# Performance work log

Measured on AMD Instinct MI355X. Metric: run time of the kernel, lower is better.

The kernel has to match this reference:

```python
import jax, jax.numpy as jnp
import numpy as np

N, E = 50000, 800000
NODE_DIM, HIDDEN, NBASIS = 128, 128, 32


def _mlp(x, w1, b1, w2, b2):
    return jax.nn.silu(x @ w1 + b1) @ w2 + b2


def setup_inputs() -> dict:
    key = jax.random.key(0)
    ks = jax.random.split(key, 16)
    d = {}
    d['h'] = jax.random.normal(ks[0], (N, NODE_DIM), dtype=jnp.float32)
    d['pos'] = jax.random.normal(ks[1], (N, 3), dtype=jnp.float32)
    d['edge_index'] = jax.random.randint(ks[2], (2, E), 0, N, dtype=jnp.int32)
    mlp_in = NODE_DIM * 2 + NBASIS
    def lin(k, fan_in, fan_out):
        bound = 1.0 / np.sqrt(fan_in)
        kw, kb = jax.random.split(k)
        w = jax.random.uniform(kw, (fan_in, fan_out), minval=-bound, maxval=bound, dtype=jnp.float32)
        b = jax.random.uniform(kb, (fan_out,), minval=-bound, maxval=bound, dtype=jnp.float32)
        return w, b
    d['mw1'], d['mb1'] = lin(ks[3], mlp_in, HIDDEN)
    d['mw2'], d['mb2'] = lin(ks[4], HIDDEN, HIDDEN)
    d['nw1'], d['nb1'] = lin(ks[5], NODE_DIM + HIDDEN, HIDDEN)
    d['nw2'], d['nb2'] = lin(ks[6], HIDDEN, NODE_DIM)
    d['cw1'], d['cb1'] = lin(ks[7], HIDDEN, HIDDEN)
    d['cw2'], d['cb2'] = lin(ks[8], HIDDEN, 1)
    return d


def reference(h, pos, edge_index, mw1, mb1, mw2, mb2, nw1, nb1, nw2, nb2, cw1, cb1, cw2, cb2):
    row, col = edge_index[0], edge_index[1]
    # Gaussian smearing constants (start=0, stop=10, num_gaussians=NBASIS)
    offset = jnp.linspace(0.0, 10.0, NBASIS)  # [NBASIS]
    coeff = -0.5 / float(10.0 / (NBASIS - 1)) ** 2

    rel_pos = pos[row] - pos[col]                       # [E, 3]
    sq_dist = jnp.sum(rel_pos ** 2, axis=1, keepdims=True)  # [E, 1]
    dist = jnp.sqrt(sq_dist + 1e-8)                     # [E, 1]
    dist_emb = jnp.exp(coeff * (dist - offset[None, :]) ** 2)  # [E, NBASIS]

    msg_in = jnp.concatenate([h[row], h[col], dist_emb], axis=1)  # [E, 2D+NBASIS]
    messages = _mlp(msg_in, mw1, mb1, mw2, mb2)         # [E, HIDDEN]

    aggr_msgs = jax.ops.segment_sum(messages, row, num_segments=h.shape[0])  # [N, HIDDEN]

    coord_mult = _mlp(messages, cw1, cb1, cw2, cb2)     # [E, 1]
    coord_updates = rel_pos * coord_mult                # [E, 3]
    aggr_coord = jax.ops.segment_sum(coord_updates, row, num_segments=pos.shape[0])
    pos_out = pos + aggr_coord

    node_in = jnp.concatenate([h, aggr_msgs], axis=1)   # [N, D+HIDDEN]
    h_out = h + _mlp(node_in, nw1, nb1, nw2, nb2)
    return (h_out, pos_out)
```

## Files before the change

kernel.cpp:

```cpp
#include <hip/hip_runtime.h>
#include <math.h>

#define N_NODES 50000
#define E_EDGES 800000
#define D 128
#define HID 128
#define NB 32
#define SCAN_BLOCKS 196

typedef __attribute__((ext_vector_type(8))) short bf16x8;
typedef __attribute__((ext_vector_type(4))) float f32x4;

#define MW1F 0
#define MW2F 72
#define CW1F 104
#define NW1F 136
#define NW2F 200
#define TOT_KSTEPS 29

__device__ __forceinline__ short f2bf(float f) {
    union { float f; unsigned u; } v; v.f = f;
    unsigned r = v.u + 0x7fffu + ((v.u >> 16) & 1u);
    return (short)(r >> 16);
}
__device__ __forceinline__ float bf2f(unsigned s) {
    union { unsigned u; float f; } v; v.u = s << 16; return v.f;
}
__device__ __forceinline__ float silu_f(float x) { return x / (1.0f + __expf(-x)); }
__device__ __forceinline__ f32x4 splat4(float b) { f32x4 v = {b, b, b, b}; return v; }

__global__ void pack_w(const float* __restrict__ mw1, const float* __restrict__ mw2,
                       const float* __restrict__ cw1, const float* __restrict__ nw1,
                       const float* __restrict__ nw2, short* __restrict__ wp)
{
    const int bid = blockIdx.x;
    const int ks = bid >> 3, nf = bid & 7;
    const int l = threadIdx.x;
    const float* src; int k0;
    if (ks < 9)       { src = mw1; k0 = ks; }
    else if (ks < 13) { src = mw2; k0 = ks - 9; }
    else if (ks < 17) { src = cw1; k0 = ks - 13; }
    else if (ks < 25) { src = nw1; k0 = ks - 17; }
    else              { src = nw2; k0 = ks - 25; }
    bf16x8 pv;
    #pragma unroll
    for (int j = 0; j < 8; ++j)
        pv[j] = f2bf(src[(size_t)(k0 * 32 + (l >> 4) * 8 + j) * 128 + nf * 16 + (l & 15)]);
    *((bf16x8*)wp + (size_t)bid * 64 + l) = pv;
}

__global__ void conv_h(const float* __restrict__ h, short* __restrict__ hb)
{
    int i = blockIdx.x * 256 + threadIdx.x;
    if (i < N_NODES * D / 8) {
        float4 va = ((const float4*)h)[i * 2];
        float4 vb = ((const float4*)h)[i * 2 + 1];
        bf16x8 o;
        o[0] = f2bf(va.x); o[1] = f2bf(va.y); o[2] = f2bf(va.z); o[3] = f2bf(va.w);
        o[4] = f2bf(vb.x); o[5] = f2bf(vb.y); o[6] = f2bf(vb.z); o[7] = f2bf(vb.w);
        ((bf16x8*)hb)[i] = o;
    }
}

__global__ void count_rows(const int* __restrict__ ei, int* __restrict__ cnt)
{
    int e = blockIdx.x * 256 + threadIdx.x;
    if (e < E_EDGES) atomicAdd(&cnt[ei[e]], 1);
}

__global__ void scan_blocks(const int* __restrict__ cnt, int* __restrict__ base,
                            int* __restrict__ bsum)
{
    __shared__ int wsum[4];
    const int t = threadIdx.x, b = blockIdx.x;
    const int i = b * 256 + t;
    int v = (i < N_NODES) ? cnt[i] : 0;
    int incl = v;
    #pragma unroll
    for (int off = 1; off < 64; off <<= 1) {
        int u = __shfl_up(incl, off);
        if ((t & 63) >= off) incl += u;
    }
    if ((t & 63) == 63) wsum[t >> 6] = incl;
    __syncthreads();
    int wo = 0;
    #pragma unroll
    for (int wv = 0; wv < 4; ++wv) if (wv < (t >> 6)) wo += wsum[wv];
    if (i < N_NODES) base[i] = wo + incl - v;
    if (t == 255) bsum[b] = wo + incl;
}

__global__ void scan_bsums(const int* __restrict__ bsum, int* __restrict__ boff)
{
    __shared__ int wsum[4];
    const int t = threadIdx.x;
    int v = (t < SCAN_BLOCKS) ? bsum[t] : 0;
    int incl = v;
    #pragma unroll
    for (int off = 1; off < 64; off <<= 1) {
        int u = __shfl_up(incl, off);
        if ((t & 63) >= off) incl += u;
    }
    if ((t & 63) == 63) wsum[t >> 6] = incl;
    __syncthreads();
    int wo = 0;
    #pragma unroll
    for (int wv = 0; wv < 4; ++wv) if (wv < (t >> 6)) wo += wsum[wv];
    if (t < SCAN_BLOCKS) boff[t] = wo + incl - v;
}

__global__ void add_offsets(int* __restrict__ base, const int* __restrict__ boff,
                            int* __restrict__ fill)
{
    int i = blockIdx.x * 256 + threadIdx.x;
    if (i < N_NODES) {
        int v = base[i] + boff[blockIdx.x];
        base[i] = v; fill[i] = v;
    }
}

__global__ void scatter_edges(const int* __restrict__ ei, int* __restrict__ fill,
                              int* __restrict__ perm)
{
    int e = blockIdx.x * 256 + threadIdx.x;
    if (e < E_EDGES) {
        int p = atomicAdd(&fill[ei[e]], 1);
        perm[p] = e;
    }
}

#define GEMM2(KSTEPS, STRIDE, WBASE)                                           \
    _Pragma("unroll")                                                          \
    for (int ks = 0; ks < KSTEPS; ++ks) {                                      \
        const int kd = ks * 32 + ag * 8;                                       \
        int b0 = ar * STRIDE + kd * 2;        b0 ^= (ar & 7) << 4;             \
        int b1 = (16 + ar) * STRIDE + kd * 2; b1 ^= (ar & 7) << 4;             \
        bf16x8 a0 = *(const bf16x8*)(sx + b0);                                 \
        bf16x8 a1 = *(const bf16x8*)(sx + b1);                                 \
        const bf16x8* bw = wpv + (size_t)(WBASE + ks * 8) * 64 + l;            \
        _Pragma("unroll")                                                      \
        for (int n = 0; n < 8; ++n) {                                          \
            bf16x8 bb = bw[n * 64];                                            \
            acc0[n] = __builtin_amdgcn_mfma_f32_16x16x32_bf16(a0, bb, acc0[n], 0, 0, 0); \
            acc1[n] = __builtin_amdgcn_mfma_f32_16x16x32_bf16(a1, bb, acc1[n], 0, 0, 0); \
        }                                                                      \
    }

template<int GATHER>
__global__ __launch_bounds__(128, 4) void egnn_edge(
    const short* __restrict__ hb, const float* __restrict__ pos,
    const int* __restrict__ ei, const int* __restrict__ perm,
    const float* __restrict__ mb1, const float* __restrict__ mb2,
    const float* __restrict__ cb1, const float* __restrict__ cw2,
    const float* __restrict__ cb2, const short* __restrict__ wp,
    float* __restrict__ aggr_msgs, float* __restrict__ aggr_coord,
    short* __restrict__ msgb, float* __restrict__ cu)
{
    __shared__ char  sm[2][8192];
    __shared__ int   s_row[2][32], s_col[2][32];
    __shared__ float s_dist[2][32];
    __shared__ float s_rel[2][32][3];

    const int t = threadIdx.x;
    const int w = t >> 6;
    const int l = t & 63;
    char* sx = sm[w];
    const bf16x8* wpv = (const bf16x8*)wp;
    const bf16x8* hbv = (const bf16x8*)hb;
    const int e0 = blockIdx.x * 64 + w * 32;

    if (l < 32) {
        const int ge = perm[e0 + l];
        const int row = ei[ge], col = ei[E_EDGES + ge];
        const float dx = pos[row * 3 + 0] - pos[col * 3 + 0];
        const float dy = pos[row * 3 + 1] - pos[col * 3 + 1];
        const float dz = pos[row * 3 + 2] - pos[col * 3 + 2];
        const float dist = sqrtf(dx * dx + dy * dy + dz * dz + 1e-8f);
        s_row[w][l] = row; s_col[w][l] = col; s_dist[w][l] = dist;
        s_rel[w][l][0] = dx; s_rel[w][l][1] = dy; s_rel[w][l][2] = dz;
    }
    asm volatile("s_waitcnt lgkmcnt(0)" ::: "memory");

    const int ar = l & 15, ag = l >> 4;
    const int row0 = s_row[w][ar],      col0 = s_col[w][ar];
    const int row1 = s_row[w][16 + ar], col1 = s_col[w][16 + ar];
    const float d0 = s_dist[w][ar], d1 = s_dist[w][16 + ar];

    const float GS = 10.0f / 31.0f;
    const float GC = -0.5f / (GS * GS);

    f32x4 acc0[8], acc1[8];

    #pragma unroll
    for (int n = 0; n < 8; ++n) {
        float b = mb1[n * 16 + ar];
        acc0[n] = splat4(b); acc1[n] = splat4(b);
    }
    #pragma unroll
    for (int ks = 0; ks < 9; ++ks) {
        bf16x8 a0, a1;
        if (ks < 4) {
            a0 = hbv[(size_t)row0 * 16 + ks * 4 + ag];
            a1 = hbv[(size_t)row1 * 16 + ks * 4 + ag];
        } else if (ks < 8) {
            a0 = hbv[(size_t)col0 * 16 + (ks - 4) * 4 + ag];
            a1 = hbv[(size_t)col1 * 16 + (ks - 4) * 4 + ag];
        } else {
            #pragma unroll
            for (int j = 0; j < 8; ++j) {
                const float g = (float)(ag * 8 + j) * GS;
                const float dd0 = d0 - g, dd1 = d1 - g;
                a0[j] = f2bf(__expf(GC * dd0 * dd0));
                a1[j] = f2bf(__expf(GC * dd1 * dd1));
            }
        }
        const bf16x8* bw = wpv + (size_t)(MW1F + ks * 8) * 64 + l;
        #pragma unroll
        for (int n = 0; n < 8; ++n) {
            bf16x8 bb = bw[n * 64];
            acc0[n] = __builtin_amdgcn_mfma_f32_16x16x32_bf16(a0, bb, acc0[n], 0, 0, 0);
            acc1[n] = __builtin_amdgcn_mfma_f32_16x16x32_bf16(a1, bb, acc1[n], 0, 0, 0);
        }
    }

    #pragma unroll
    for (int m = 0; m < 2; ++m)
        #pragma unroll
        for (int n = 0; n < 8; ++n)
            #pragma unroll
            for (int r = 0; r < 4; ++r) {
                float x = (m == 0) ? acc0[n][r] : acc1[n][r];
                const int rw = m * 16 + ag * 4 + r;
                const int cl = n * 16 + ar;
                int byte = rw * 256 + cl * 2;
                byte ^= (rw & 7) << 4;
                *(short*)(sx + byte) = f2bf(silu_f(x));
            }
    asm volatile("s_waitcnt lgkmcnt(0)" ::: "memory");

    #pragma unroll
    for (int n = 0; n < 8; ++n) {
        float b = mb2[n * 16 + ar];
        acc0[n] = splat4(b); acc1[n] = splat4(b);
    }
    GEMM2(4, 256, MW2F)

    int grows[2][4];
    #pragma unroll
    for (int m = 0; m < 2; ++m)
        #pragma unroll
        for (int r = 0; r < 4; ++r)
            grows[m][r] = s_row[w][m * 16 + ag * 4 + r];

    #pragma unroll
    for (int m = 0; m < 2; ++m)
        #pragma unroll
        for (int n = 0; n < 8; ++n)
            #pragma unroll
            for (int r = 0; r < 4; ++r) {
                float x = (m == 0) ? acc0[n][r] : acc1[n][r];
                const int rw = m * 16 + ag * 4 + r;
                const int cl = n * 16 + ar;
                int byte = rw * 256 + cl * 2;
                byte ^= (rw & 7) << 4;
                *(short*)(sx + byte) = f2bf(x);
            }
    asm volatile("s_waitcnt lgkmcnt(0)" ::: "memory");

    if (GATHER) {
        #pragma unroll
        for (int p = 0; p < 8; ++p) {
            const int rw = p * 4 + (l >> 4);
            int byte = rw * 256 + (l & 15) * 16;
            byte ^= (rw & 7) << 4;
            bf16x8 v = *(const bf16x8*)(sx + byte);
            *(bf16x8*)(msgb + (size_t)(e0 + rw) * D + (l & 15) * 8) = v;
        }
    } else {
        #pragma unroll
        for (int m = 0; m < 2; ++m)
            #pragma unroll
            for (int n = 0; n < 8; ++n) {
                const int cl = n * 16 + ar;
                float s = (m == 0) ? acc0[n][0] : acc1[n][0];
                #pragma unroll
                for (int r = 0; r < 3; ++r) {
                    float nxt = (m == 0) ? acc0[n][r + 1] : acc1[n][r + 1];
                    if (grows[m][r + 1] == grows[m][r]) s += nxt;
                    else {
                        atomicAdd(&aggr_msgs[(size_t)grows[m][r] * D + cl], s);
                        s = nxt;
                    }
                }
                atomicAdd(&aggr_msgs[(size_t)grows[m][3] * D + cl], s);
            }
    }

    #pragma unroll
    for (int n = 0; n < 8; ++n) {
        float b = cb1[n * 16 + ar];
        acc0[n] = splat4(b); acc1[n] = splat4(b);
    }
    GEMM2(4, 256, CW1F)

    float cw2v[8];
    #pragma unroll
    for (int n = 0; n < 8; ++n) cw2v[n] = cw2[n * 16 + ar];
    float p0[4], p1[4];
    #pragma unroll
    for (int r = 0; r < 4; ++r) {
        float s0 = 0.f, s1 = 0.f;
        #pragma unroll
        for (int n = 0; n < 8; ++n) {
            s0 += silu_f(acc0[n][r]) * cw2v[n];
            s1 += silu_f(acc1[n][r]) * cw2v[n];
        }
        p0[r] = s0; p1[r] = s1;
    }
    #pragma unroll
    for (int off = 1; off < 16; off <<= 1) {
        #pragma unroll
        for (int r = 0; r < 4; ++r) {
            p0[r] += __shfl_xor(p0[r], off);
            p1[r] += __shfl_xor(p1[r], off);
        }
    }
    if (ar == 0) {
        const float cb = cb2[0];
        if (GATHER) {
            #pragma unroll
            for (int m = 0; m < 2; ++m)
                #pragma unroll
                for (int r = 0; r < 4; ++r) {
                    const int el = m * 16 + ag * 4 + r;
                    const float mm = ((m == 0) ? p0[r] : p1[r]) + cb;
                    float* dst = cu + (size_t)(e0 + el) * 3;
                    dst[0] = s_rel[w][el][0] * mm;
                    dst[1] = s_rel[w][el][1] * mm;
                    dst[2] = s_rel[w][el][2] * mm;
                }
        } else {
            #pragma unroll
            for (int m = 0; m < 2; ++m) {
                float cx = 0.f, cy = 0.f, cz = 0.f;
                #pragma unroll
                for (int r = 0; r < 4; ++r) {
                    const int el = m * 16 + ag * 4 + r;
                    const float mm = ((m == 0) ? p0[r] : p1[r]) + cb;
                    cx += s_rel[w][el][0] * mm;
                    cy += s_rel[w][el][1] * mm;
                    cz += s_rel[w][el][2] * mm;
                    const bool last = (r == 3) || (grows[m][r + 1] != grows[m][r]);
                    if (last) {
                        const int gr = grows[m][r];
                        atomicAdd(&aggr_coord[gr * 3 + 0], cx);
                        atomicAdd(&aggr_coord[gr * 3 + 1], cy);
                        atomicAdd(&aggr_coord[gr * 3 + 2], cz);
                        cx = 0.f; cy = 0.f; cz = 0.f;
                    }
                }
            }
        }
    }
}

__global__ __launch_bounds__(256) void aggr_gather(
    const short* __restrict__ msgb, const int* __restrict__ base,
    const int* __restrict__ fill, float* __restrict__ aggr)
{
    const int node = blockIdx.x * 4 + (threadIdx.x >> 6);
    if (node >= N_NODES) return;
    const int l = threadIdx.x & 63;
    const int b = base[node], e = fill[node];
    const unsigned* mv = (const unsigned*)msgb;
    float a0 = 0.f, a1 = 0.f;
    for (int i = b; i < e; ++i) {
        unsigned v = mv[(size_t)i * 64 + l];
        a0 += bf2f(v & 0xffffu);
        a1 += bf2f(v >> 16);
    }
    float2 o; o.x = a0; o.y = a1;
    *(float2*)(aggr + (size_t)node * D + l * 2) = o;
}

__global__ void coord_pos(const float* __restrict__ pos, const float* __restrict__ cu,
                          const int* __restrict__ base, const int* __restrict__ fill,
                          float* __restrict__ pout)
{
    int n = blockIdx.x * 256 + threadIdx.x;
    if (n < N_NODES) {
        const int b = base[n], e = fill[n];
        float ax = 0.f, ay = 0.f, az = 0.f;
        for (int i = b; i < e; ++i) {
            ax += cu[(size_t)i * 3 + 0];
            ay += cu[(size_t)i * 3 + 1];
            az += cu[(size_t)i * 3 + 2];
        }
        pout[n * 3 + 0] = pos[n * 3 + 0] + ax;
        pout[n * 3 + 1] = pos[n * 3 + 1] + ay;
        pout[n * 3 + 2] = pos[n * 3 + 2] + az;
    }
}

__global__ __launch_bounds__(128, 2) void egnn_node(
    const float* __restrict__ h, const float* __restrict__ aggr,
    const float* __restrict__ nb1, const float* __restrict__ nb2,
    const short* __restrict__ wp, float* __restrict__ out)
{
    __shared__ char sm[2][16384];
    const int t = threadIdx.x, w = t >> 6, l = t & 63;
    char* sx = sm[w];
    const bf16x8* wpv = (const bf16x8*)wp;
    const int n0 = blockIdx.x * 64 + w * 32;

    {
        const int n_loc = l & 31, half = l >> 5;
        int gn = n0 + n_loc; if (gn >= N_NODES) gn = N_NODES - 1;
        const float* src = (half == 0) ? (h + (size_t)gn * D) : (aggr + (size_t)gn * D);
        #pragma unroll
        for (int c = 0; c < 16; ++c) {
            float4 va = *(const float4*)(src + c * 8);
            float4 vb = *(const float4*)(src + c * 8 + 4);
            float v[8] = {va.x, va.y, va.z, va.w, vb.x, vb.y, vb.z, vb.w};
            bf16x8 sv;
            #pragma unroll
            for (int j = 0; j < 8; ++j) sv[j] = f2bf(v[j]);
            int byte = n_loc * 512 + (half * 128 + c * 8) * 2;
            byte ^= (n_loc & 7) << 4;
            *(bf16x8*)(sx + byte) = sv;
        }
    }
    asm volatile("s_waitcnt lgkmcnt(0)" ::: "memory");

    const int ar = l & 15, ag = l >> 4;
    f32x4 acc0[8], acc1[8];

    #pragma unroll
    for (int n = 0; n < 8; ++n) {
        float b = nb1[n * 16 + ar];
        acc0[n] = splat4(b); acc1[n] = splat4(b);
    }
    GEMM2(8, 512, NW1F)

    #pragma unroll
    for (int m = 0; m < 2; ++m)
        #pragma unroll
        for (int n = 0; n < 8; ++n)
            #pragma unroll
            for (int r = 0; r < 4; ++r) {
                float x = (m == 0) ? acc0[n][r] : acc1[n][r];
                const int rw = m * 16 + ag * 4 + r;
                const int cl = n * 16 + ar;
                int byte = rw * 256 + cl * 2;
                byte ^= (rw & 7) << 4;
                *(short*)(sx + byte) = f2bf(silu_f(x));
            }
    asm volatile("s_waitcnt lgkmcnt(0)" ::: "memory");

    #pragma unroll
    for (int n = 0; n < 8; ++n) {
        float b = nb2[n * 16 + ar];
        acc0[n] = splat4(b); acc1[n] = splat4(b);
    }
    GEMM2(4, 256, NW2F)

    #pragma unroll
    for (int m = 0; m < 2; ++m)
        #pragma unroll
        for (int n = 0; n < 8; ++n)
            #pragma unroll
            for (int r = 0; r < 4; ++r) {
                const int rw = m * 16 + ag * 4 + r;
                const int gnode = n0 + rw;
                if (gnode < N_NODES) {
                    const int cl = n * 16 + ar;
                    float x = (m == 0) ? acc0[n][r] : acc1[n][r];
                    out[(size_t)gnode * D + cl] = h[(size_t)gnode * D + cl] + x;
                }
            }
}

__global__ void egnn_pos(const float* __restrict__ pos,
                         const float* __restrict__ aggr_coord,
                         float* __restrict__ pout)
{
    int i = blockIdx.x * 256 + threadIdx.x;
    if (i < N_NODES * 3) pout[i] = pos[i] + aggr_coord[i];
}

extern "C" void kernel_launch(void* const* d_in, const int* in_sizes, int n_in,
                              void* d_out, int out_size, void* d_ws, size_t ws_size,
                              hipStream_t stream)
{
    const float* h   = (const float*)d_in[0];
    const float* pos = (const float*)d_in[1];
    const int*   ei  = (const int*)d_in[2];
    const float* mw1 = (const float*)d_in[3];
    const float* mb1 = (const float*)d_in[4];
    const float* mw2 = (const float*)d_in[5];
    const float* mb2 = (const float*)d_in[6];
    const float* nw1 = (const float*)d_in[7];
    const float* nb1 = (const float*)d_in[8];
    const float* nw2 = (const float*)d_in[9];
    const float* nb2 = (const float*)d_in[10];
    const float* cw1 = (const float*)d_in[11];
    const float* cb1 = (const float*)d_in[12];
    const float* cw2 = (const float*)d_in[13];
    const float* cb2 = (const float*)d_in[14];

    float* out = (float*)d_out;
    char*  ws  = (char*)d_ws;

    size_t o = 0;
    #define WALLOC(name, bytes) size_t name = o; o = (o + (size_t)(bytes) + 15) & ~(size_t)15;
    WALLOC(o_aggrm, (size_t)N_NODES * D * 4)
    WALLOC(o_aggrc, (size_t)N_NODES * 3 * 4)
    WALLOC(o_wpack, (size_t)TOT_KSTEPS * 8 * 64 * 8 * 2)
    WALLOC(o_hb,    (size_t)N_NODES * D * 2)
    WALLOC(o_cnt,   (size_t)N_NODES * 4)
    WALLOC(o_base,  (size_t)N_NODES * 4)
    WALLOC(o_fill,  (size_t)N_NODES * 4)
    WALLOC(o_bsum,  256 * 4)
    WALLOC(o_boff,  256 * 4)
    WALLOC(o_perm,  (size_t)E_EDGES * 4)
    WALLOC(o_msgb,  (size_t)E_EDGES * D * 2)
    WALLOC(o_cu,    (size_t)E_EDGES * 3 * 4)
    const size_t needed = o;
    #undef WALLOC

    float* aggr_msgs  = (float*)(ws + o_aggrm);
    float* aggr_coord = (float*)(ws + o_aggrc);
    short* wpack      = (short*)(ws + o_wpack);
    short* hb         = (short*)(ws + o_hb);
    int*   cnt        = (int*)(ws + o_cnt);
    int*   base       = (int*)(ws + o_base);
    int*   fill       = (int*)(ws + o_fill);
    int*   bsum       = (int*)(ws + o_bsum);
    int*   boff       = (int*)(ws + o_boff);
    int*   perm       = (int*)(ws + o_perm);
    short* msgb       = (short*)(ws + o_msgb);
    float* cu         = (float*)(ws + o_cu);

    const bool gather = (ws_size >= needed);

    hipMemsetAsync(cnt, 0, (size_t)N_NODES * sizeof(int), stream);
    if (!gather)
        hipMemsetAsync(aggr_msgs, 0,
                       (size_t)(N_NODES * D + N_NODES * 3) * sizeof(float), stream);

    pack_w<<<TOT_KSTEPS * 8, 64, 0, stream>>>(mw1, mw2, cw1, nw1, nw2, wpack);
    conv_h<<<(N_NODES * D / 8 + 255) / 256, 256, 0, stream>>>(h, hb);

    count_rows<<<(E_EDGES + 255) / 256, 256, 0, stream>>>(ei, cnt);
    scan_blocks<<<SCAN_BLOCKS, 256, 0, stream>>>(cnt, base, bsum);
    scan_bsums<<<1, 256, 0, stream>>>(bsum, boff);
    add_offsets<<<SCAN_BLOCKS, 256, 0, stream>>>(base, boff, fill);
    scatter_edges<<<(E_EDGES + 255) / 256, 256, 0, stream>>>(ei, fill, perm);

    if (gather) {
        egnn_edge<1><<<E_EDGES / 64, 128, 0, stream>>>(
            hb, pos, ei, perm, mb1, mb2, cb1, cw2, cb2, wpack,
            aggr_msgs, aggr_coord, msgb, cu);
        aggr_gather<<<(N_NODES + 3) / 4, 256, 0, stream>>>(msgb, base, fill, aggr_msgs);
        egnn_node<<<(N_NODES + 63) / 64, 128, 0, stream>>>(
            h, aggr_msgs, nb1, nb2, wpack, out);
        coord_pos<<<(N_NODES + 255) / 256, 256, 0, stream>>>(
            pos, cu, base, fill, out + (size_t)N_NODES * D);
    } else {
        egnn_edge<0><<<E_EDGES / 64, 128, 0, stream>>>(
            hb, pos, ei, perm, mb1, mb2, cb1, cw2, cb2, wpack,
            aggr_msgs, aggr_coord, msgb, cu);
        egnn_node<<<(N_NODES + 63) / 64, 128, 0, stream>>>(
            h, aggr_msgs, nb1, nb2, wpack, out);
        egnn_pos<<<(N_NODES * 3 + 255) / 256, 256, 0, stream>>>(
            pos, aggr_coord, out + (size_t)N_NODES * D);
    }
}
```

Before: 628.7 us.

## Fuse message aggregation into node MLP kernel and merge prep kernels

Folds the per-node CSR gather of bf16 messages into the node MLP kernel, writing the summed aggregate straight into shared memory as bf16. This drops the separate aggr_gather launch and the fp32 aggregate round trip through global memory. It also merges the h-to-bf16 conversion and the row-count atomics into one prep kernel, and restructures the coord atomic flush loop. The trade-off is less parallelism in the gather: one wave now walks 32 nodes serially instead of one wave per node, which could lengthen the node kernel.

```diff
diff --git a/kernel.cpp b/kernel.cpp
--- a/kernel.cpp
+++ b/kernel.cpp
@@ -49,7 +49,8 @@
     *((bf16x8*)wp + (size_t)bid * 64 + l) = pv;
 }
 
-__global__ void conv_h(const float* __restrict__ h, short* __restrict__ hb)
+__global__ void prep(const float* __restrict__ h, const int* __restrict__ ei,
+                     short* __restrict__ hb, int* __restrict__ cnt)
 {
     int i = blockIdx.x * 256 + threadIdx.x;
     if (i < N_NODES * D / 8) {
@@ -60,12 +61,7 @@
         o[4] = f2bf(vb.x); o[5] = f2bf(vb.y); o[6] = f2bf(vb.z); o[7] = f2bf(vb.w);
         ((bf16x8*)hb)[i] = o;
     }
-}
-
-__global__ void count_rows(const int* __restrict__ ei, int* __restrict__ cnt)
-{
-    int e = blockIdx.x * 256 + threadIdx.x;
-    if (e < E_EDGES) atomicAdd(&cnt[ei[e]], 1);
+    if (i < E_EDGES) atomicAdd(&cnt[ei[i]], 1);
 }
 
 __global__ void scan_blocks(const int* __restrict__ cnt, int* __restrict__ base,
@@ -333,8 +329,9 @@
                 #pragma unroll
                 for (int r = 0; r < 4; ++r) {
                     const int el = m * 16 + ag * 4 + r;
+                    const int ge = e0 + el;
                     const float mm = ((m == 0) ? p0[r] : p1[r]) + cb;
-                    float* dst = cu + (size_t)(e0 + el) * 3;
+                    float* dst = cu + (size_t)ge * 3;
                     dst[0] = s_rel[w][el][0] * mm;
                     dst[1] = s_rel[w][el][1] * mm;
                     dst[2] = s_rel[w][el][2] * mm;
@@ -343,44 +340,133 @@
             #pragma unroll
             for (int m = 0; m < 2; ++m) {
                 float cx = 0.f, cy = 0.f, cz = 0.f;
+                int rprev = grows[m][0];
                 #pragma unroll
                 for (int r = 0; r < 4; ++r) {
                     const int el = m * 16 + ag * 4 + r;
+                    const int gr = grows[m][r];
                     const float mm = ((m == 0) ? p0[r] : p1[r]) + cb;
+                    if (gr != rprev) {
+                        atomicAdd(&aggr_coord[rprev * 3 + 0], cx);
+                        atomicAdd(&aggr_coord[rprev * 3 + 1], cy);
+                        atomicAdd(&aggr_coord[rprev * 3 + 2], cz);
+                        cx = 0.f; cy = 0.f; cz = 0.f; rprev = gr;
+                    }
                     cx += s_rel[w][el][0] * mm;
                     cy += s_rel[w][el][1] * mm;
                     cz += s_rel[w][el][2] * mm;
-                    const bool last = (r == 3) || (grows[m][r + 1] != grows[m][r]);
-                    if (last) {
-                        const int gr = grows[m][r];
-                        atomicAdd(&aggr_coord[gr * 3 + 0], cx);
-                        atomicAdd(&aggr_coord[gr * 3 + 1], cy);
-                        atomicAdd(&aggr_coord[gr * 3 + 2], cz);
-                        cx = 0.f; cy = 0.f; cz = 0.f;
-                    }
                 }
-            }
-        }
-    }
-}
-
-__global__ __launch_bounds__(256) void aggr_gather(
+                atomicAdd(&aggr_coord[rprev * 3 + 0], cx);
+                atomicAdd(&aggr_coord[rprev * 3 + 1], cy);
+                atomicAdd(&aggr_coord[rprev * 3 + 2], cz);
+            }
+        }
+    }
+}
+
+template<int GATHER>
+__global__ __launch_bounds__(128, 2) void egnn_node(
+    const float* __restrict__ h, const float* __restrict__ aggrf,
     const short* __restrict__ msgb, const int* __restrict__ base,
-    const int* __restrict__ fill, float* __restrict__ aggr)
-{
-    const int node = blockIdx.x * 4 + (threadIdx.x >> 6);
-    if (node >= N_NODES) return;
-    const int l = threadIdx.x & 63;
-    const int b = base[node], e = fill[node];
-    const unsigned* mv = (const unsigned*)msgb;
-    float a0 = 0.f, a1 = 0.f;
-    for (int i = b; i < e; ++i) {
-        unsigned v = mv[(size_t)i * 64 + l];
-        a0 += bf2f(v & 0xffffu);
-        a1 += bf2f(v >> 16);
-    }
-    float2 o; o.x = a0; o.y = a1;
-    *(float2*)(aggr + (size_t)node * D + l * 2) = o;
+    const int* __restrict__ fill,
+    const float* __restrict__ nb1, const float* __restrict__ nb2,
+    const short* __restrict__ wp, float* __restrict__ out)
+{
+    __shared__ char sm[2][16384];
+    const int t = threadIdx.x, w = t >> 6, l = t & 63;
+    char* sx = sm[w];
+    const bf16x8* wpv = (const bf16x8*)wp;
+    const int n0 = blockIdx.x * 64 + w * 32;
+
+    {
+        const int n_loc = l & 31, half = l >> 5;
+        int gn = n0 + n_loc; if (gn >= N_NODES) gn = N_NODES - 1;
+        const bool do_stage = GATHER ? (half == 0) : true;
+        if (do_stage) {
+            const float* src = (half == 0) ? (h + (size_t)gn * D)
+                                           : (aggrf + (size_t)gn * D);
+            #pragma unroll
+            for (int c = 0; c < 16; ++c) {
+                float4 va = *(const float4*)(src + c * 8);
+                float4 vb = *(const float4*)(src + c * 8 + 4);
+                float v[8] = {va.x, va.y, va.z, va.w, vb.x, vb.y, vb.z, vb.w};
+                bf16x8 sv;
+                #pragma unroll
+                for (int j = 0; j < 8; ++j) sv[j] = f2bf(v[j]);
+                int byte = n_loc * 512 + (half * 128 + c * 8) * 2;
+                byte ^= (n_loc & 7) << 4;
+                *(bf16x8*)(sx + byte) = sv;
+            }
+        }
+    }
+
+    if (GATHER) {
+        const unsigned* mv = (const unsigned*)msgb;
+        for (int nl = 0; nl < 32; ++nl) {
+            const int gn2 = n0 + nl;
+            float a0 = 0.f, a1 = 0.f;
+            if (gn2 < N_NODES) {
+                const int b = base[gn2], e = fill[gn2];
+                for (int i = b; i < e; ++i) {
+                    unsigned v = mv[(size_t)i * 64 + l];
+                    a0 += bf2f(v & 0xffffu);
+                    a1 += bf2f(v >> 16);
+                }
+            }
+            int byte = nl * 512 + 256 + l * 4;
+            byte ^= (nl & 7) << 4;
+            *(short*)(sx + byte)     = f2bf(a0);
+            *(short*)(sx + byte + 2) = f2bf(a1);
+        }
+    }
+    asm volatile("s_waitcnt lgkmcnt(0)" ::: "memory");
+
+    const int ar = l & 15, ag = l >> 4;
+    f32x4 acc0[8], acc1[8];
+
+    #pragma unroll
+    for (int n = 0; n < 8; ++n) {
+        float b = nb1[n * 16 + ar];
+        acc0[n] = splat4(b); acc1[n] = splat4(b);
+    }
+    GEMM2(8, 512, NW1F)
+
+    #pragma unroll
+    for (int m = 0; m < 2; ++m)
+        #pragma unroll
+        for (int n = 0; n < 8; ++n)
+            #pragma unroll
+            for (int r = 0; r < 4; ++r) {
+                float x = (m == 0) ? acc0[n][r] : acc1[n][r];
+                const int rw = m * 16 + ag * 4 + r;
+                const int cl = n * 16 + ar;
+                int byte = rw * 256 + cl * 2;
+                byte ^= (rw & 7) << 4;
+                *(short*)(sx + byte) = f2bf(silu_f(x));
+            }
+    asm volatile("s_waitcnt lgkmcnt(0)" ::: "memory");
+
+    #pragma unroll
+    for (int n = 0; n < 8; ++n) {
+        float b = nb2[n * 16 + ar];
+        acc0[n] = splat4(b); acc1[n] = splat4(b);
+    }
+    GEMM2(4, 256, NW2F)
+
+    #pragma unroll
+    for (int m = 0; m < 2; ++m)
+        #pragma unroll
+        for (int n = 0; n < 8; ++n)
+            #pragma unroll
+            for (int r = 0; r < 4; ++r) {
+                const int rw = m * 16 + ag * 4 + r;
+                const int gnode = n0 + rw;
+                if (gnode < N_NODES) {
+                    const int cl = n * 16 + ar;
+                    float x = (m == 0) ? acc0[n][r] : acc1[n][r];
+                    out[(size_t)gnode * D + cl] = h[(size_t)gnode * D + cl] + x;
+                }
+            }
 }
 
 __global__ void coord_pos(const float* __restrict__ pos, const float* __restrict__ cu,
@@ -400,84 +486,6 @@
         pout[n * 3 + 1] = pos[n * 3 + 1] + ay;
         pout[n * 3 + 2] = pos[n * 3 + 2] + az;
     }
-}
-
-__global__ __launch_bounds__(128, 2) void egnn_node(
-    const float* __restrict__ h, const float* __restrict__ aggr,
-    const float* __restrict__ nb1, const float* __restrict__ nb2,
-    const short* __restrict__ wp, float* __restrict__ out)
-{
-    __shared__ char sm[2][16384];
-    const int t = threadIdx.x, w = t >> 6, l = t & 63;
-    char* sx = sm[w];
-    const bf16x8* wpv = (const bf16x8*)wp;
-    const int n0 = blockIdx.x * 64 + w * 32;
-
-    {
-        const int n_loc = l & 31, half = l >> 5;
-        int gn = n0 + n_loc; if (gn >= N_NODES) gn = N_NODES - 1;
-        const float* src = (half == 0) ? (h + (size_t)gn * D) : (aggr + (size_t)gn * D);
-        #pragma unroll
-        for (int c = 0; c < 16; ++c) {
-            float4 va = *(const float4*)(src + c * 8);
-            float4 vb = *(const float4*)(src + c * 8 + 4);
-            float v[8] = {va.x, va.y, va.z, va.w, vb.x, vb.y, vb.z, vb.w};
-            bf16x8 sv;
-            #pragma unroll
-            for (int j = 0; j < 8; ++j) sv[j] = f2bf(v[j]);
-            int byte = n_loc * 512 + (half * 128 + c * 8) * 2;
-            byte ^= (n_loc & 7) << 4;
-            *(bf16x8*)(sx + byte) = sv;
-        }
-    }
-    asm volatile("s_waitcnt lgkmcnt(0)" ::: "memory");
-
-    const int ar = l & 15, ag = l >> 4;
-    f32x4 acc0[8], acc1[8];
-
-    #pragma unroll
-    for (int n = 0; n < 8; ++n) {
-        float b = nb1[n * 16 + ar];
-        acc0[n] = splat4(b); acc1[n] = splat4(b);
-    }
-    GEMM2(8, 512, NW1F)
-
-    #pragma unroll
-    for (int m = 0; m < 2; ++m)
-        #pragma unroll
-        for (int n = 0; n < 8; ++n)
-            #pragma unroll
-            for (int r = 0; r < 4; ++r) {
-                float x = (m == 0) ? acc0[n][r] : acc1[n][r];
-                const int rw = m * 16 + ag * 4 + r;
-                const int cl = n * 16 + ar;
-                int byte = rw * 256 + cl * 2;
-                byte ^= (rw & 7) << 4;
-                *(short*)(sx + byte) = f2bf(silu_f(x));
-            }
-    asm volatile("s_waitcnt lgkmcnt(0)" ::: "memory");
-
-    #pragma unroll
-    for (int n = 0; n < 8; ++n) {
-        float b = nb2[n * 16 + ar];
-        acc0[n] = splat4(b); acc1[n] = splat4(b);
-    }
-    GEMM2(4, 256, NW2F)
-
-    #pragma unroll
-    for (int m = 0; m < 2; ++m)
-        #pragma unroll
-        for (int n = 0; n < 8; ++n)
-            #pragma unroll
-            for (int r = 0; r < 4; ++r) {
-                const int rw = m * 16 + ag * 4 + r;
-                const int gnode = n0 + rw;
-                if (gnode < N_NODES) {
-                    const int cl = n * 16 + ar;
-                    float x = (m == 0) ? acc0[n][r] : acc1[n][r];
-                    out[(size_t)gnode * D + cl] = h[(size_t)gnode * D + cl] + x;
-                }
-            }
 }
 
 __global__ void egnn_pos(const float* __restrict__ pos,
@@ -549,9 +557,8 @@
                        (size_t)(N_NODES * D + N_NODES * 3) * sizeof(float), stream);
 
     pack_w<<<TOT_KSTEPS * 8, 64, 0, stream>>>(mw1, mw2, cw1, nw1, nw2, wpack);
-    conv_h<<<(N_NODES * D / 8 + 255) / 256, 256, 0, stream>>>(h, hb);
-
-    count_rows<<<(E_EDGES + 255) / 256, 256, 0, stream>>>(ei, cnt);
+    prep<<<(E_EDGES + 255) / 256, 256, 0, stream>>>(h, ei, hb, cnt);
+
     scan_blocks<<<SCAN_BLOCKS, 256, 0, stream>>>(cnt, base, bsum);
     scan_bsums<<<1, 256, 0, stream>>>(bsum, boff);
     add_offsets<<<SCAN_BLOCKS, 256, 0, stream>>>(base, boff, fill);
@@ -561,17 +568,16 @@
         egnn_edge<1><<<E_EDGES / 64, 128, 0, stream>>>(
             hb, pos, ei, perm, mb1, mb2, cb1, cw2, cb2, wpack,
             aggr_msgs, aggr_coord, msgb, cu);
-        aggr_gather<<<(N_NODES + 3) / 4, 256, 0, stream>>>(msgb, base, fill, aggr_msgs);
-        egnn_node<<<(N_NODES + 63) / 64, 128, 0, stream>>>(
-            h, aggr_msgs, nb1, nb2, wpack, out);
+        egnn_node<1><<<(N_NODES + 63) / 64, 128, 0, stream>>>(
+            h, aggr_msgs, msgb, base, fill, nb1, nb2, wpack, out);
         coord_pos<<<(N_NODES + 255) / 256, 256, 0, stream>>>(
             pos, cu, base, fill, out + (size_t)N_NODES * D);
     } else {
         egnn_edge<0><<<E_EDGES / 64, 128, 0, stream>>>(
             hb, pos, ei, perm, mb1, mb2, cb1, cw2, cb2, wpack,
             aggr_msgs, aggr_coord, msgb, cu);
-        egnn_node<<<(N_NODES + 63) / 64, 128, 0, stream>>>(
-            h, aggr_msgs, nb1, nb2, wpack, out);
+        egnn_node<0><<<(N_NODES + 63) / 64, 128, 0, stream>>>(
+            h, aggr_msgs, msgb, base, fill, nb1, nb2, wpack, out);
         egnn_pos<<<(N_NODES * 3 + 255) / 256, 256, 0, stream>>>(
             pos, aggr_coord, out + (size_t)N_NODES * D);
     }
```

Measured after the change: 780.2 us. 1.24x slower.
